# Optimization experiments

Measured on AMD Instinct MI355X. Metric: run time of the kernel, lower is better.

## Reference

```python
import jax, jax.numpy as jnp
import numpy as np

N = 100000      # nodes
E = 1600000     # edges (avg degree 16)
IN_FEATS = 128
HEADS = 4
OUT_FEATS = 16
NEG_SLOPE = 0.2
EPS = 1e-16


def setup_inputs() -> dict:
    key = jax.random.key(0)
    k1, k2, k3, k4, k5, k6 = jax.random.split(key, 6)
    feat = jax.random.normal(k1, (N, IN_FEATS), dtype=jnp.float32)
    # xavier-ish scale for params
    W = jax.random.normal(k2, (IN_FEATS, HEADS * OUT_FEATS), dtype=jnp.float32) * 0.1
    attn_l = jax.random.normal(k3, (1, HEADS, OUT_FEATS), dtype=jnp.float32) * 0.1
    attn_r = jax.random.normal(k4, (1, HEADS, OUT_FEATS), dtype=jnp.float32) * 0.1
    src_index = jax.random.randint(k5, (E,), 0, N, dtype=jnp.int32)
    trg_index = jax.random.randint(k6, (E,), 0, N, dtype=jnp.int32)
    return {"feat": feat, "W": W, "attn_l": attn_l, "attn_r": attn_r,
            "src_index": src_index, "trg_index": trg_index}


def reference(feat, W, attn_l, attn_r, src_index, trg_index):
    # dropout layers are identity in eval mode
    n = feat.shape[0]
    h = (feat @ W).reshape(n, HEADS, OUT_FEATS)            # [N,H,F]
    el = jnp.sum(h * attn_l, axis=-1)                      # [N,H]
    er = jnp.sum(h * attn_r, axis=-1)                      # [N,H]
    s = el[src_index] + er[trg_index]                      # [E,H] edge scores
    s = jnp.where(s > 0, s, NEG_SLOPE * s)                 # LeakyReLU(0.2)
    # neighborhood-aware softmax over incoming edges of each target node
    s = s - jnp.max(s)                                     # global max shift (as in source)
    e = jnp.exp(s)                                         # [E,H]
    denom = jax.ops.segment_sum(e, trg_index, num_segments=n)  # [N,H]
    attn = e / (denom[trg_index] + EPS)                    # [E,H]
    # weighted aggregation of lifted source features into target nodes
    msg = h[src_index] * attn[:, :, None]                  # [E,H,F]
    h_prime = jax.ops.segment_sum(msg, trg_index, num_segments=n)  # [N,H,F]
    return h_prime.reshape(n, HEADS * OUT_FEATS)
```

## Files before the change

### kernel.cpp

```cpp
#include <hip/hip_runtime.h>

typedef unsigned short ushort_t;
typedef __attribute__((ext_vector_type(8))) short bf16x8;
typedef __attribute__((ext_vector_type(4))) float f32x4v;

#define BN 128
#define LOGBN 7
#define CAP 3072
#define MAXBKT 1024

static __device__ __forceinline__ ushort_t f2bf(float f) {
  union { float f; unsigned int i; } v; v.f = f;
  unsigned int r = v.i + 0x7FFFu + ((v.i >> 16) & 1u);
  return (ushort_t)(r >> 16);
}
static __device__ __forceinline__ float leaky(float s) {
  return s > 0.f ? s : 0.2f * s;
}

__global__ __launch_bounds__(256) void packw_hist(
    const float* __restrict__ W, const float* __restrict__ attnl,
    const float* __restrict__ attnr, ushort_t* __restrict__ wfrag,
    const int* __restrict__ trg, int E, int nbkt,
    int* __restrict__ blockHist, int nb3, int epb)
{
  const int b = blockIdx.x;
  const int t = threadIdx.x;
  if (b == nb3) {
    __shared__ float sW[128 * 64];
    __shared__ float sAl[64], sAr[64];
    for (int i = t; i < 128 * 64 / 4; i += 256)
      ((float4*)sW)[i] = ((const float4*)W)[i];
    if (t < 64) sAl[t] = attnl[t];
    else if (t < 128) sAr[t - 64] = attnr[t - 64];
    __syncthreads();
    const int kc = t >> 6, l = t & 63;
    const int q = l >> 4, n = l & 15;
    #pragma unroll
    for (int tile = 0; tile < 5; ++tile) {
      #pragma unroll
      for (int j = 0; j < 8; ++j) {
        const int k = kc * 32 + q * 8 + j;
        float v = 0.f;
        if (tile < 4) {
          v = sW[k * 64 + tile * 16 + n];
        } else if (n < 4) {
          for (int f = 0; f < 16; ++f)
            v += sW[k * 64 + n * 16 + f] * sAl[n * 16 + f];
        } else if (n < 8) {
          const int hd = n - 4;
          for (int f = 0; f < 16; ++f)
            v += sW[k * 64 + hd * 16 + f] * sAr[hd * 16 + f];
        }
        wfrag[((tile * 4 + kc) * 64 + l) * 8 + j] = f2bf(v);
      }
    }
    return;
  }
  __shared__ int hist[MAXBKT];
  for (int i = t; i < nbkt; i += 256) hist[i] = 0;
  __syncthreads();
  const int start = b * epb;
  const int end = min(start + epb, E);
  for (int e = start + t; e < end; e += 256)
    atomicAdd(&hist[trg[e] >> LOGBN], 1);
  __syncthreads();
  for (int i = t; i < nbkt; i += 256) blockHist[b * nbkt + i] = hist[i];
}

__global__ __launch_bounds__(64) void bucket_scan(
    int* __restrict__ blockHist, int nb3, int nbkt, int* __restrict__ colTotal)
{
  const int b = blockIdx.x;
  const int l = threadIdx.x;
  int carry = 0;
  for (int r = 0; r * 64 < nb3; ++r) {
    const int i = r * 64 + l;
    int v = (i < nb3) ? blockHist[i * nbkt + b] : 0;
    int incl = v;
    #pragma unroll
    for (int d = 1; d < 64; d <<= 1) {
      int u = __shfl_up(incl, d, 64);
      if (l >= d) incl += u;
    }
    if (i < nb3) blockHist[i * nbkt + b] = carry + incl - v;
    carry += __shfl(incl, 63, 64);
  }
  if (l == 0) colTotal[b] = carry;
}

__global__ __launch_bounds__(64) void bucket_base(
    const int* __restrict__ colTotal, int nbkt, int* __restrict__ bucketBase)
{
  const int l = threadIdx.x;
  int carry = 0;
  for (int r = 0; r * 64 < nbkt; ++r) {
    const int i = r * 64 + l;
    int v = (i < nbkt) ? colTotal[i] : 0;
    int incl = v;
    #pragma unroll
    for (int d = 1; d < 64; d <<= 1) {
      int u = __shfl_up(incl, d, 64);
      if (l >= d) incl += u;
    }
    if (i < nbkt) bucketBase[i] = carry + incl - v;
    carry += __shfl(incl, 63, 64);
  }
  if (l == 0) bucketBase[nbkt] = carry;
}

__global__ __launch_bounds__(256) void bucket_scatter(
    const int* __restrict__ src, const int* __restrict__ trg, int E, int nbkt,
    const int* __restrict__ blockHist, const int* __restrict__ bucketBase,
    unsigned int* __restrict__ binned, int epb)
{
  __shared__ int cursor[MAXBKT];
  const int t = threadIdx.x, b = blockIdx.x;
  for (int i = t; i < nbkt; i += 256)
    cursor[i] = bucketBase[i] + blockHist[b * nbkt + i];
  __syncthreads();
  const int start = b * epb;
  const int end = min(start + epb, E);
  for (int e = start + t; e < end; e += 256) {
    const int ti = trg[e];
    const int bkt = ti >> LOGBN;
    const int pos = atomicAdd(&cursor[bkt], 1);
    binned[pos] = ((unsigned int)src[e] << LOGBN) | (unsigned int)(ti & (BN - 1));
  }
}

__global__ __launch_bounds__(256) void gat_linear(
    const float* __restrict__ feat, const ushort_t* __restrict__ wfrag,
    ushort_t* __restrict__ h_out, float* __restrict__ el, float* __restrict__ er,
    float* __restrict__ blockmax2, int N)
{
  __shared__ ushort_t sFb[64 * 136];
  __shared__ float wmax[8];
  const int t = threadIdx.x;
  const int b = blockIdx.x;
  const int w = t >> 6, l = t & 63;
  const int q = l >> 4, m = l & 15;

  const float4* gF = (const float4*)(feat + (size_t)b * 64 * 128);
  #pragma unroll
  for (int i = 0; i < 8; ++i) {
    const int idx = i * 256 + t;
    const int node = idx >> 5, off = idx & 31;
    float4 v = make_float4(0.f, 0.f, 0.f, 0.f);
    if (b * 64 + node < N) v = gF[idx];
    unsigned int p0 = ((unsigned int)f2bf(v.y) << 16) | f2bf(v.x);
    unsigned int p1 = ((unsigned int)f2bf(v.w) << 16) | f2bf(v.z);
    *(uint2*)(sFb + node * 136 + off * 4) = make_uint2(p0, p1);
  }
  __syncthreads();

  bf16x8 a[4];
  const ushort_t* arow = sFb + (w * 16 + m) * 136 + q * 8;
  #pragma unroll
  for (int kc = 0; kc < 4; ++kc)
    a[kc] = *(const bf16x8*)(arow + kc * 32);

  #pragma unroll
  for (int tile = 0; tile < 4; ++tile) {
    f32x4v acc = {0.f, 0.f, 0.f, 0.f};
    #pragma unroll
    for (int kc = 0; kc < 4; ++kc) {
      bf16x8 bfr = *(const bf16x8*)(wfrag + ((tile * 4 + kc) * 64 + l) * 8);
      acc = __builtin_amdgcn_mfma_f32_16x16x32_bf16(a[kc], bfr, acc, 0, 0, 0);
    }
    #pragma unroll
    for (int r = 0; r < 4; ++r) {
      const int gn = b * 64 + w * 16 + q * 4 + r;
      if (gn < N) h_out[(size_t)gn * 64 + tile * 16 + m] = f2bf(acc[r]);
    }
  }

  f32x4v acc4 = {0.f, 0.f, 0.f, 0.f};
  #pragma unroll
  for (int kc = 0; kc < 4; ++kc) {
    bf16x8 bfr = *(const bf16x8*)(wfrag + ((4 * 4 + kc) * 64 + l) * 8);
    acc4 = __builtin_amdgcn_mfma_f32_16x16x32_bf16(a[kc], bfr, acc4, 0, 0, 0);
  }
  float mel = -1e30f, mer = -1e30f;
  #pragma unroll
  for (int r = 0; r < 4; ++r) {
    const int gn = b * 64 + w * 16 + q * 4 + r;
    const float v = acc4[r];
    if (m < 4) {
      if (gn < N) el[gn * 4 + m] = v;
      mel = fmaxf(mel, v);
    } else if (m < 8) {
      if (gn < N) er[gn * 4 + (m - 4)] = v;
      mer = fmaxf(mer, v);
    }
  }
  #pragma unroll
  for (int o = 1; o <= 32; o <<= 1) {
    mel = fmaxf(mel, __shfl_xor(mel, o, 64));
    mer = fmaxf(mer, __shfl_xor(mer, o, 64));
  }
  if (l == 0) { wmax[w * 2] = mel; wmax[w * 2 + 1] = mer; }
  __syncthreads();
  if (t == 0) {
    float aa = fmaxf(fmaxf(wmax[0], wmax[2]), fmaxf(wmax[4], wmax[6]));
    float cc = fmaxf(fmaxf(wmax[1], wmax[3]), fmaxf(wmax[5], wmax[7]));
    blockmax2[b * 2] = aa;
    blockmax2[b * 2 + 1] = cc;
  }
}

__global__ __launch_bounds__(256) void fine_sort(
    unsigned int* __restrict__ binned, const int* __restrict__ bucketBase,
    int* __restrict__ rowbeg, int* __restrict__ rowend, int N,
    const float* __restrict__ blockmax2, int nbL, float* __restrict__ gmaxM)
{
  __shared__ unsigned int pld[CAP];
  __shared__ int hist[BN];
  __shared__ int cursor[BN];
  __shared__ int wtot[2];
  __shared__ float wmg[8];
  const int t = threadIdx.x;
  const int b = blockIdx.x;
  const int base = bucketBase[b];
  const int cn = min(bucketBase[b + 1] - base, CAP);
  unsigned int* slot = binned + base;

  if (t < BN) hist[t] = 0;
  if (b == 0) {
    const int l = t & 63, w = t >> 6;
    float mel = -1e30f, mer = -1e30f;
    for (int i = t; i < nbL; i += 256) {
      mel = fmaxf(mel, blockmax2[i * 2]);
      mer = fmaxf(mer, blockmax2[i * 2 + 1]);
    }
    #pragma unroll
    for (int o = 1; o <= 32; o <<= 1) {
      mel = fmaxf(mel, __shfl_xor(mel, o, 64));
      mer = fmaxf(mer, __shfl_xor(mer, o, 64));
    }
    if (l == 0) { wmg[w * 2] = mel; wmg[w * 2 + 1] = mer; }
  }
  __syncthreads();
  if (b == 0 && t == 0) {
    float aa = fmaxf(fmaxf(wmg[0], wmg[2]), fmaxf(wmg[4], wmg[6]));
    float cc = fmaxf(fmaxf(wmg[1], wmg[3]), fmaxf(wmg[5], wmg[7]));
    gmaxM[0] = fmaxf(0.f, aa + cc);
  }
  for (int i = t; i < cn; i += 256) {
    const unsigned int pv = slot[i];
    pld[i] = pv;
    atomicAdd(&hist[pv & (BN - 1)], 1);
  }
  __syncthreads();

  int v = 0, incl = 0;
  if (t < BN) {
    v = hist[t];
    incl = v;
    #pragma unroll
    for (int d = 1; d < 64; d <<= 1) {
      int u = __shfl_up(incl, d, 64);
      if ((t & 63) >= d) incl += u;
    }
  }
  if (t < BN && (t & 63) == 63) wtot[t >> 6] = incl;
  __syncthreads();
  if (t < BN) {
    const int excl = incl - v + ((t >= 64) ? wtot[0] : 0);
    cursor[t] = excl;
    const int node = b * BN + t;
    if (node < N) {
      rowbeg[node] = base + excl;
      rowend[node] = base + excl + v;
    }
  }
  __syncthreads();

  for (int i = t; i < cn; i += 256) {
    const unsigned int pv = pld[i];
    const int pos = atomicAdd(&cursor[pv & (BN - 1)], 1);
    slot[pos] = pv >> LOGBN;
  }
}

#define UNPACK_FMA(hv, p, acc) do { \
  union { unsigned int i; float f; } c_; \
  c_.i = (hv).x << 16;          acc[0] += c_.f * (p); \
  c_.i = (hv).x & 0xffff0000u;  acc[1] += c_.f * (p); \
  c_.i = (hv).y << 16;          acc[2] += c_.f * (p); \
  c_.i = (hv).y & 0xffff0000u;  acc[3] += c_.f * (p); \
  c_.i = (hv).z << 16;          acc[4] += c_.f * (p); \
  c_.i = (hv).z & 0xffff0000u;  acc[5] += c_.f * (p); \
  c_.i = (hv).w << 16;          acc[6] += c_.f * (p); \
  c_.i = (hv).w & 0xffff0000u;  acc[7] += c_.f * (p); \
} while (0)

#define LOADJ(j, hA_, hB_, qA_, qB_) do { \
  const int i_ = iA0 + (j) * 4; \
  const int sA_ = sSw[i_]; \
  const int sB_ = sSw[i_ + 32]; \
  qA_ = sPw[i_ * 4 + hd2]; \
  qB_ = sPw[(i_ + 32) * 4 + hd2]; \
  hA_ = *(const uint4*)(hcg + (size_t)sA_ * 64); \
  hB_ = *(const uint4*)(hcg + (size_t)sB_ * 64); \
} while (0)

__global__ __launch_bounds__(256) void gat_agg(
    const unsigned int* __restrict__ csrsrc, const int* __restrict__ rowbeg,
    const int* __restrict__ rowend,
    const float4* __restrict__ el4, const float4* __restrict__ er4,
    const ushort_t* __restrict__ hbf, const float* __restrict__ gmaxM,
    float* __restrict__ out, int N)
{
  __shared__ float sP[4 * 64 * 4];
  __shared__ int sS[4 * 64];
  const int t = threadIdx.x;
  const int l = t & 63;
  const int w = t >> 6;
  const int nbase = blockIdx.x * 16 + w * 4;
  const int rg = l >> 3;
  const int cg = l & 7;
  const int hd2 = cg >> 1;
  const int ks = l >> 4;
  const int le = l & 15;
  const float M = gmaxM[0];
  float* sPw = sP + w * 256;
  int* sSw = sS + w * 64;
  const ushort_t* hcg = hbf + cg * 8;
  const int iA0 = ((rg >> 2) * 16) + (rg & 3);

  const int nk = nbase + ks;
  int rs = 0, re = 0;
  if (nk < N) { rs = rowbeg[nk]; re = rowend[nk]; }
  const float4 ernk = (rs < re) ? er4[nk]
                                : make_float4(0.f, 0.f, 0.f, 0.f);
  int deg = re - rs;
  deg = max(deg, __shfl_xor(deg, 16, 64));
  deg = max(deg, __shfl_xor(deg, 32, 64));
  const int chunks = (deg + 15) >> 4;

  float aA[8] = {0.f,0.f,0.f,0.f,0.f,0.f,0.f,0.f};
  float aB[8] = {0.f,0.f,0.f,0.f,0.f,0.f,0.f,0.f};
  float dA = 0.f, dB = 0.f;

  for (int c = 0; c < chunks; ++c) {
    int sn = 0;
    float4 pv = make_float4(0.f, 0.f, 0.f, 0.f);
    const int ei = rs + c * 16 + le;
    if (ei < re) {
      sn = (int)csrsrc[ei];
      const float4 a = el4[sn];
      pv.x = __expf(leaky(a.x + ernk.x) - M);
      pv.y = __expf(leaky(a.y + ernk.y) - M);
      pv.z = __expf(leaky(a.z + ernk.z) - M);
      pv.w = __expf(leaky(a.w + ernk.w) - M);
    }
    *(float4*)(sPw + l * 4) = pv;
    sSw[l] = sn;

    const int rem = min(deg - c * 16, 16);
    const int jmax = (rem + 3) >> 2;
    uint4 h0A, h0B, h1A, h1B, h2A, h2B, h3A, h3B;
    float q0A, q0B, q1A, q1B, q2A, q2B, q3A, q3B;
    LOADJ(0, h0A, h0B, q0A, q0B);
    if (jmax > 1) LOADJ(1, h1A, h1B, q1A, q1B);
    if (jmax > 2) LOADJ(2, h2A, h2B, q2A, q2B);
    if (jmax > 3) LOADJ(3, h3A, h3B, q3A, q3B);

    UNPACK_FMA(h0A, q0A, aA); UNPACK_FMA(h0B, q0B, aB);
    dA += q0A; dB += q0B;
    if (jmax > 1) {
      UNPACK_FMA(h1A, q1A, aA); UNPACK_FMA(h1B, q1B, aB);
      dA += q1A; dB += q1B;
    }
    if (jmax > 2) {
      UNPACK_FMA(h2A, q2A, aA); UNPACK_FMA(h2B, q2B, aB);
      dA += q2A; dB += q2B;
    }
    if (jmax > 3) {
      UNPACK_FMA(h3A, q3A, aA); UNPACK_FMA(h3B, q3B, aB);
      dA += q3A; dB += q3B;
    }
  }

  #pragma unroll
  for (int o = 8; o <= 16; o <<= 1) {
    #pragma unroll
    for (int i = 0; i < 8; ++i) {
      aA[i] += __shfl_xor(aA[i], o, 64);
      aB[i] += __shfl_xor(aB[i], o, 64);
    }
    dA += __shfl_xor(dA, o, 64);
    dB += __shfl_xor(dB, o, 64);
  }
  if ((rg & 3) == 0) {
    const int nA = nbase + (rg >> 2);
    const int nB = nA + 2;
    const float rA = 1.0f / (dA + 1e-16f);
    const float rB = 1.0f / (dB + 1e-16f);
    if (nA < N) {
      float4* orow = (float4*)(out + (size_t)nA * 64 + cg * 8);
      orow[0] = make_float4(aA[0] * rA, aA[1] * rA, aA[2] * rA, aA[3] * rA);
      orow[1] = make_float4(aA[4] * rA, aA[5] * rA, aA[6] * rA, aA[7] * rA);
    }
    if (nB < N) {
      float4* orow = (float4*)(out + (size_t)nB * 64 + cg * 8);
      orow[0] = make_float4(aB[0] * rB, aB[1] * rB, aB[2] * rB, aB[3] * rB);
      orow[1] = make_float4(aB[4] * rB, aB[5] * rB, aB[6] * rB, aB[7] * rB);
    }
  }
}

extern "C" void kernel_launch(void* const* d_in, const int* in_sizes, int n_in,
                              void* d_out, int out_size, void* d_ws, size_t ws_size,
                              hipStream_t stream) {
  const float* feat  = (const float*)d_in[0];
  const float* W     = (const float*)d_in[1];
  const float* attnl = (const float*)d_in[2];
  const float* attnr = (const float*)d_in[3];
  const int* src = (const int*)d_in[4];
  const int* trg = (const int*)d_in[5];
  float* out = (float*)d_out;

  const int N = in_sizes[0] / 128;
  const int E = in_sizes[4];

  const int nbL  = (N + 63) / 64;
  const int nbkt = (N + BN - 1) >> LOGBN;
  const int nb3  = 256;
  const int epb  = (E + nb3 - 1) / nb3;

  char* p = (char*)d_ws;
  auto take = [&](size_t bytes) -> char* {
    char* r = p;
    p += (bytes + 255) & ~(size_t)255;
    return r;
  };
  ushort_t* h_bf  = (ushort_t*)take((size_t)N * 64 * 2);
  float* el       = (float*)take((size_t)N * 16);
  float* er       = (float*)take((size_t)N * 16);
  unsigned int* binned = (unsigned int*)take((size_t)E * 4);
  int* rowbeg     = (int*)take((size_t)N * 4);
  int* rowend     = (int*)take((size_t)N * 4);
  ushort_t* wfrag = (ushort_t*)take(5 * 4 * 64 * 8 * 2);
  int* blockHist  = (int*)take((size_t)nb3 * nbkt * 4);
  int* colTotal   = (int*)take((size_t)nbkt * 4);
  int* bucketBase = (int*)take((size_t)(nbkt + 1) * 4);
  float* blockmax2 = (float*)take((size_t)nbL * 2 * 4);
  float* gmaxM    = (float*)take(256);

  packw_hist<<<nb3 + 1, 256, 0, stream>>>(W, attnl, attnr, wfrag,
                                          trg, E, nbkt, blockHist, nb3, epb);
  gat_linear<<<nbL, 256, 0, stream>>>(feat, wfrag, h_bf, el, er,
                                      blockmax2, N);
  bucket_scan<<<nbkt, 64, 0, stream>>>(blockHist, nb3, nbkt, colTotal);
  bucket_base<<<1, 64, 0, stream>>>(colTotal, nbkt, bucketBase);
  bucket_scatter<<<nb3, 256, 0, stream>>>(src, trg, E, nbkt, blockHist,
                                          bucketBase, binned, epb);
  fine_sort<<<nbkt, 256, 0, stream>>>(binned, bucketBase, rowbeg, rowend, N,
                                      blockmax2, nbL, gmaxM);
  gat_agg<<<(N + 15) / 16, 256, 0, stream>>>(binned, rowbeg, rowend,
                                             (const float4*)el,
                                             (const float4*)er, h_bf,
                                             gmaxM, out, N);
}
```

Measured before the change: 220.7 us.

## Fold bucket scans into linear and scatter kernels to cut launches

The per-bucket column scan now runs as extra blocks appended to the linear-projection kernel, each using one 256-thread block per bucket instead of a 64-thread serial loop. The bucket-base prefix scan over column totals is recomputed redundantly in every scatter block, and block 0 writes bucketBase. This drops two kernel launches, reducing launch and dependency overhead, at the cost of redundant scan work in every scatter block and a hardcoded NB3 of 256.

```diff
diff --git a/kernel.cpp b/kernel.cpp
--- a/kernel.cpp
+++ b/kernel.cpp
@@ -8,6 +8,7 @@
 #define LOGBN 7
 #define CAP 3072
 #define MAXBKT 1024
+#define NB3 256
 
 static __device__ __forceinline__ ushort_t f2bf(float f) {
   union { float f; unsigned int i; } v; v.f = f;
@@ -22,11 +23,11 @@
     const float* __restrict__ W, const float* __restrict__ attnl,
     const float* __restrict__ attnr, ushort_t* __restrict__ wfrag,
     const int* __restrict__ trg, int E, int nbkt,
-    int* __restrict__ blockHist, int nb3, int epb)
+    int* __restrict__ blockHist, int epb)
 {
   const int b = blockIdx.x;
   const int t = threadIdx.x;
-  if (b == nb3) {
+  if (b == NB3) {
     __shared__ float sW[128 * 64];
     __shared__ float sAl[64], sAr[64];
     for (int i = t; i < 128 * 64 / 4; i += 256)
@@ -68,79 +69,38 @@
   for (int i = t; i < nbkt; i += 256) blockHist[b * nbkt + i] = hist[i];
 }
 
-__global__ __launch_bounds__(64) void bucket_scan(
-    int* __restrict__ blockHist, int nb3, int nbkt, int* __restrict__ colTotal)
+__global__ __launch_bounds__(256) void linear_scan(
+    const float* __restrict__ feat, const ushort_t* __restrict__ wfrag,
+    ushort_t* __restrict__ h_out, float* __restrict__ el, float* __restrict__ er,
+    float* __restrict__ blockmax2, int N, int nbL,
+    int* __restrict__ blockHist, int nbkt, int* __restrict__ colTotal)
 {
+  __shared__ ushort_t sFb[64 * 136];
+  __shared__ float wmax[8];
+  __shared__ int wt[4];
+  const int t = threadIdx.x;
   const int b = blockIdx.x;
-  const int l = threadIdx.x;
-  int carry = 0;
-  for (int r = 0; r * 64 < nb3; ++r) {
-    const int i = r * 64 + l;
-    int v = (i < nb3) ? blockHist[i * nbkt + b] : 0;
+  const int w = t >> 6, l = t & 63;
+
+  if (b >= nbL) {
+    const int sb = b - nbL;
+    const int v = blockHist[t * nbkt + sb];
     int incl = v;
     #pragma unroll
     for (int d = 1; d < 64; d <<= 1) {
       int u = __shfl_up(incl, d, 64);
       if (l >= d) incl += u;
     }
-    if (i < nb3) blockHist[i * nbkt + b] = carry + incl - v;
-    carry += __shfl(incl, 63, 64);
-  }
-  if (l == 0) colTotal[b] = carry;
-}
-
-__global__ __launch_bounds__(64) void bucket_base(
-    const int* __restrict__ colTotal, int nbkt, int* __restrict__ bucketBase)
-{
-  const int l = threadIdx.x;
-  int carry = 0;
-  for (int r = 0; r * 64 < nbkt; ++r) {
-    const int i = r * 64 + l;
-    int v = (i < nbkt) ? colTotal[i] : 0;
-    int incl = v;
-    #pragma unroll
-    for (int d = 1; d < 64; d <<= 1) {
-      int u = __shfl_up(incl, d, 64);
-      if (l >= d) incl += u;
-    }
-    if (i < nbkt) bucketBase[i] = carry + incl - v;
-    carry += __shfl(incl, 63, 64);
-  }
-  if (l == 0) bucketBase[nbkt] = carry;
-}
-
-__global__ __launch_bounds__(256) void bucket_scatter(
-    const int* __restrict__ src, const int* __restrict__ trg, int E, int nbkt,
-    const int* __restrict__ blockHist, const int* __restrict__ bucketBase,
-    unsigned int* __restrict__ binned, int epb)
-{
-  __shared__ int cursor[MAXBKT];
-  const int t = threadIdx.x, b = blockIdx.x;
-  for (int i = t; i < nbkt; i += 256)
-    cursor[i] = bucketBase[i] + blockHist[b * nbkt + i];
-  __syncthreads();
-  const int start = b * epb;
-  const int end = min(start + epb, E);
-  for (int e = start + t; e < end; e += 256) {
-    const int ti = trg[e];
-    const int bkt = ti >> LOGBN;
-    const int pos = atomicAdd(&cursor[bkt], 1);
-    binned[pos] = ((unsigned int)src[e] << LOGBN) | (unsigned int)(ti & (BN - 1));
-  }
-}
-
-__global__ __launch_bounds__(256) void gat_linear(
-    const float* __restrict__ feat, const ushort_t* __restrict__ wfrag,
-    ushort_t* __restrict__ h_out, float* __restrict__ el, float* __restrict__ er,
-    float* __restrict__ blockmax2, int N)
-{
-  __shared__ ushort_t sFb[64 * 136];
-  __shared__ float wmax[8];
-  const int t = threadIdx.x;
-  const int b = blockIdx.x;
-  const int w = t >> 6, l = t & 63;
+    if (l == 63) wt[w] = incl;
+    __syncthreads();
+    int woff = 0;
+    for (int k = 0; k < w; ++k) woff += wt[k];
+    blockHist[t * nbkt + sb] = woff + incl - v;
+    if (t == 255) colTotal[sb] = woff + incl;
+    return;
+  }
+
   const int q = l >> 4, m = l & 15;
-
   const float4* gF = (const float4*)(feat + (size_t)b * 64 * 128);
   #pragma unroll
   for (int i = 0; i < 8; ++i) {
@@ -206,6 +166,51 @@
     float cc = fmaxf(fmaxf(wmax[1], wmax[3]), fmaxf(wmax[5], wmax[7]));
     blockmax2[b * 2] = aa;
     blockmax2[b * 2 + 1] = cc;
+  }
+}
+
+__global__ __launch_bounds__(256) void bucket_scatter(
+    const int* __restrict__ src, const int* __restrict__ trg, int E, int nbkt,
+    const int* __restrict__ blockHist, const int* __restrict__ colTotal,
+    unsigned int* __restrict__ binned, int epb, int* __restrict__ bucketBase)
+{
+  __shared__ int cursor[MAXBKT];
+  __shared__ int wt[4];
+  const int t = threadIdx.x, b = blockIdx.x;
+  const int l = t & 63, w = t >> 6;
+
+  int carry = 0;
+  for (int ch = 0; ch * 256 < nbkt; ++ch) {
+    const int i = ch * 256 + t;
+    const int v = (i < nbkt) ? colTotal[i] : 0;
+    int incl = v;
+    #pragma unroll
+    for (int d = 1; d < 64; d <<= 1) {
+      int u = __shfl_up(incl, d, 64);
+      if (l >= d) incl += u;
+    }
+    if (l == 63) wt[w] = incl;
+    __syncthreads();
+    int woff = 0;
+    for (int k = 0; k < w; ++k) woff += wt[k];
+    if (i < nbkt) cursor[i] = carry + woff + incl - v;
+    carry += wt[0] + wt[1] + wt[2] + wt[3];
+    __syncthreads();
+  }
+  if (b == 0) {
+    for (int i = t; i < nbkt; i += 256) bucketBase[i] = cursor[i];
+    if (t == 0) bucketBase[nbkt] = carry;
+  }
+  for (int i = t; i < nbkt; i += 256) cursor[i] += blockHist[b * nbkt + i];
+  __syncthreads();
+
+  const int start = b * epb;
+  const int end = min(start + epb, E);
+  for (int e = start + t; e < end; e += 256) {
+    const int ti = trg[e];
+    const int bkt = ti >> LOGBN;
+    const int pos = atomicAdd(&cursor[bkt], 1);
+    binned[pos] = ((unsigned int)src[e] << LOGBN) | (unsigned int)(ti & (BN - 1));
   }
 }
 
@@ -427,8 +432,7 @@
 
   const int nbL  = (N + 63) / 64;
   const int nbkt = (N + BN - 1) >> LOGBN;
-  const int nb3  = 256;
-  const int epb  = (E + nb3 - 1) / nb3;
+  const int epb  = (E + NB3 - 1) / NB3;
 
   char* p = (char*)d_ws;
   auto take = [&](size_t bytes) -> char* {
@@ -443,20 +447,19 @@
   int* rowbeg     = (int*)take((size_t)N * 4);
   int* rowend     = (int*)take((size_t)N * 4);
   ushort_t* wfrag = (ushort_t*)take(5 * 4 * 64 * 8 * 2);
-  int* blockHist  = (int*)take((size_t)nb3 * nbkt * 4);
+  int* blockHist  = (int*)take((size_t)NB3 * nbkt * 4);
   int* colTotal   = (int*)take((size_t)nbkt * 4);
   int* bucketBase = (int*)take((size_t)(nbkt + 1) * 4);
   float* blockmax2 = (float*)take((size_t)nbL * 2 * 4);
   float* gmaxM    = (float*)take(256);
 
-  packw_hist<<<nb3 + 1, 256, 0, stream>>>(W, attnl, attnr, wfrag,
-                                          trg, E, nbkt, blockHist, nb3, epb);
-  gat_linear<<<nbL, 256, 0, stream>>>(feat, wfrag, h_bf, el, er,
-                                      blockmax2, N);
-  bucket_scan<<<nbkt, 64, 0, stream>>>(blockHist, nb3, nbkt, colTotal);
-  bucket_base<<<1, 64, 0, stream>>>(colTotal, nbkt, bucketBase);
-  bucket_scatter<<<nb3, 256, 0, stream>>>(src, trg, E, nbkt, blockHist,
-                                          bucketBase, binned, epb);
+  packw_hist<<<NB3 + 1, 256, 0, stream>>>(W, attnl, attnr, wfrag,
+                                          trg, E, nbkt, blockHist, epb);
+  linear_scan<<<nbL + nbkt, 256, 0, stream>>>(feat, wfrag, h_bf, el, er,
+                                              blockmax2, N, nbL,
+                                              blockHist, nbkt, colTotal);
+  bucket_scatter<<<NB3, 256, 0, stream>>>(src, trg, E, nbkt, blockHist,
+                                          colTotal, binned, epb, bucketBase);
   fine_sort<<<nbkt, 256, 0, stream>>>(binned, bucketBase, rowbeg, rowend, N,
                                       blockmax2, nbL, gmaxM);
   gat_agg<<<(N + 15) / 16, 256, 0, stream>>>(binned, rowbeg, rowend,
```

Result: faster. 210.1 us (-4.8%).
